# Kernel optimization log

Measured on AMD Instinct MI355X. Metric: run time of the kernel, lower is better.

Reference implementation:

```python
import jax, jax.numpy as jnp
import numpy as np

N, E, G = 40000, 640000, 64
D, H, O = 128, 128, 10
EPS = 1e-5


def _lin(k, fan_in, shape):
    b = 1.0 / np.sqrt(fan_in)
    return jax.random.uniform(k, shape, jnp.float32, -b, b)


def setup_inputs() -> dict:
    key = jax.random.key(0)
    ks = jax.random.split(key, 12)
    x = jax.random.normal(ks[0], (N, D), jnp.float32)
    edge_index = jax.random.randint(ks[1], (2, E), 0, N)
    batch = jnp.sort(jax.random.randint(ks[2], (N,), 0, G))
    return {
        "x": x,
        "edge_index": edge_index,
        "batch": batch,
        "num_graphs": G,
        "W_gcn": _lin(ks[3], D, (D, H)),
        "b_gcn": jnp.zeros((H,), jnp.float32),
        "gamma": jnp.ones((H,), jnp.float32),
        "beta": jnp.zeros((H,), jnp.float32),
        "W1": _lin(ks[4], 3 * H, (3 * H, H)),
        "b1": _lin(ks[5], 3 * H, (H,)),
        "W2": _lin(ks[6], H, (H, H // 2)),
        "b2": _lin(ks[7], H, (H // 2,)),
        "W3": _lin(ks[8], H // 2, (H // 2, O)),
        "b3": _lin(ks[9], H // 2, (O,)),
    }


def reference(x, edge_index, batch, num_graphs, W_gcn, b_gcn, gamma, beta, W1, b1, W2, b2, W3, b3):
    n = x.shape[0]
    src, dst = edge_index[0], edge_index[1]
    # GCNConv: h = D^{-1/2} (A + I) D^{-1/2} (x W) + b  (self-loops, symmetric norm)
    h = x @ W_gcn                                   # [N, H]
    deg = jax.ops.segment_sum(jnp.ones((src.shape[0],), h.dtype), dst, num_segments=n) + 1.0
    dinv = jax.lax.rsqrt(deg)                       # [N]
    coef = dinv[src] * dinv[dst]                    # [E]
    msg = h[src] * coef[:, None]                    # [E, H] gather (memory bound)
    agg = jax.ops.segment_sum(msg, dst, num_segments=n)
    agg = agg + h * (dinv * dinv)[:, None] + b_gcn  # self-loop term + bias
    h = jax.nn.relu(agg)
    # LayerNorm over feature dim
    mu = jnp.mean(h, axis=-1, keepdims=True)
    var = jnp.mean(jnp.square(h - mu), axis=-1, keepdims=True)
    h = (h - mu) * jax.lax.rsqrt(var + EPS) * gamma + beta
    # global mean / add / max pools keyed by graph id
    counts = jax.ops.segment_sum(jnp.ones((n,), h.dtype), batch, num_segments=num_graphs)
    x_add = jax.ops.segment_sum(h, batch, num_segments=num_graphs)
    x_mean = x_add / jnp.maximum(counts, 1.0)[:, None]
    x_max = jax.ops.segment_max(h, batch, num_segments=num_graphs)
    x_max = jnp.where(counts[:, None] > 0, x_max, 0.0)
    g = jnp.concatenate([x_mean, x_add, x_max], axis=1)  # [G, 3H]
    # MLP head (dropout is identity at inference)
    g = jax.nn.relu(g @ W1 + b1)
    g = jax.nn.relu(g @ W2 + b2)
    return g @ W3 + b3
```

## Files before the change

kernel.cpp:

```cpp
#include <hip/hip_runtime.h>
#include <math.h>

#define EPS 1e-5f
#define FLT_BIG 3.402823466e38f

typedef __attribute__((ext_vector_type(8))) short bf16x8;
typedef __attribute__((ext_vector_type(4))) float f32x4;

__device__ __forceinline__ unsigned fflip(float f){
  int i = __float_as_int(f);
  return (unsigned)(i ^ ((i>>31) | 0x80000000));
}
__device__ __forceinline__ float funflip(unsigned u){
  int i = (u & 0x80000000u) ? (int)(u ^ 0x80000000u) : (int)(~u);
  return __int_as_float(i);
}
__device__ __forceinline__ unsigned f2bf(float f){
  unsigned u = __float_as_uint(f);
  return (u + 0x7FFFu + ((u>>16)&1u)) >> 16;
}
__device__ __forceinline__ float bf_lo(unsigned v){ return __uint_as_float(v<<16); }
__device__ __forceinline__ float bf_hi(unsigned v){ return __uint_as_float(v & 0xFFFF0000u); }

__device__ __forceinline__ int lbound(const int* __restrict__ a, int n, int key){
  int lo=0, hi=n;
  while(lo<hi){ int mid=(lo+hi)>>1; if(a[mid]<key) lo=mid+1; else hi=mid; }
  return lo;
}

__global__ __launch_bounds__(256) void k_init(
    int* __restrict__ cursor, int N,
    unsigned* __restrict__ psum, unsigned* __restrict__ pmaxu, int GP,
    const float* __restrict__ Wg, ushort* __restrict__ Wp,
    const int* __restrict__ batch, int* __restrict__ gcnt, int G){
  int i = blockIdx.x*blockDim.x + threadIdx.x;
  if(i<N) cursor[i] = 0;
  if(i<GP){ psum[i]=0u; pmaxu[i]=0u; }
  if(i<G){
    int s = lbound(batch,N,i), e = lbound(batch,N,i+1);
    gcnt[i] = e - s;
  }
  if(i<2048){
    int tile = i>>6, l = i&63;
    int kt = tile>>3, ct = tile&7;
    int q = l>>4, nn = l&15;
    ushort w8[8];
    #pragma unroll
    for(int j=0;j<8;j++)
      w8[j] = (ushort)f2bf(Wg[(kt*32 + q*8 + j)*128 + ct*16 + nn]);
    ushort* dst = Wp + (size_t)i*8;
    #pragma unroll
    for(int j=0;j<8;j++) dst[j] = w8[j];
  }
}

__global__ void k_scatter(const int* __restrict__ src, const int* __restrict__ dst, int E,
                          int* __restrict__ cursor, ushort* __restrict__ csr){
  int i = blockIdx.x*blockDim.x + threadIdx.x;
  int e = i<<2;
  if((E&3)==0){
    if(e<E){
      int4 s4 = *(const int4*)(src+e);
      int4 d4 = *(const int4*)(dst+e);
      int p;
      p = atomicAdd(&cursor[d4.x],1); if(p<64) csr[(d4.x<<6)+p] = (ushort)s4.x;
      p = atomicAdd(&cursor[d4.y],1); if(p<64) csr[(d4.y<<6)+p] = (ushort)s4.y;
      p = atomicAdd(&cursor[d4.z],1); if(p<64) csr[(d4.z<<6)+p] = (ushort)s4.z;
      p = atomicAdd(&cursor[d4.w],1); if(p<64) csr[(d4.w<<6)+p] = (ushort)s4.w;
    }
  } else {
    #pragma unroll
    for(int j=0;j<4;j++){
      int ee = e+j;
      if(ee<E){
        int s = src[ee], d = dst[ee];
        int p = atomicAdd(&cursor[d],1);
        if(p<64) csr[(d<<6)+p] = (ushort)s;
      }
    }
  }
}

__global__ __launch_bounds__(256) void k_scale(
    const float4* __restrict__ x4, int nq, const int* __restrict__ cursor,
    uint2* __restrict__ xs2){
  int i = blockIdx.x*blockDim.x + threadIdx.x;
  if(i>=nq) return;
  int node = i>>5;
  int deg = cursor[node]; if(deg>64) deg=64;
  float dinv = rsqrtf((float)deg + 1.0f);
  float4 v = x4[i];
  uint2 o;
  o.x = (f2bf(v.y*dinv)<<16) | f2bf(v.x*dinv);
  o.y = (f2bf(v.w*dinv)<<16) | f2bf(v.z*dinv);
  xs2[i] = o;
}

__global__ void k_agg(const uint4* __restrict__ xs4, const int* __restrict__ cursor,
                      const ushort* __restrict__ csr, int n, uint4* __restrict__ zb4){
  int w = (blockIdx.x*blockDim.x + threadIdx.x)>>6;
  if(w>=n) return;
  int lane = threadIdx.x & 63;
  int grp = lane>>4, li = lane&15;
  int deg = cursor[w]; if(deg>64) deg=64;
  int k0 = w<<6, k1 = k0+deg;
  float dd = rsqrtf((float)deg + 1.0f);
  float a0=0.f,a1=0.f,a2=0.f,a3=0.f,a4=0.f,a5=0.f,a6=0.f,a7=0.f;
  if(grp==0){
    uint4 sv = xs4[(w<<4)+li];
    a0=bf_lo(sv.x); a1=bf_hi(sv.x); a2=bf_lo(sv.y); a3=bf_hi(sv.y);
    a4=bf_lo(sv.z); a5=bf_hi(sv.z); a6=bf_lo(sv.w); a7=bf_hi(sv.w);
  }
  for(int kb=k0; kb<k1; kb+=16){
    int base = kb + (grp<<2);
    ushort4 s4 = *(const ushort4*)(csr + base);
    if(base   < k1){ uint4 v = xs4[((int)s4.x<<4)+li];
      a0+=bf_lo(v.x); a1+=bf_hi(v.x); a2+=bf_lo(v.y); a3+=bf_hi(v.y);
      a4+=bf_lo(v.z); a5+=bf_hi(v.z); a6+=bf_lo(v.w); a7+=bf_hi(v.w); }
    if(base+1 < k1){ uint4 v = xs4[((int)s4.y<<4)+li];
      a0+=bf_lo(v.x); a1+=bf_hi(v.x); a2+=bf_lo(v.y); a3+=bf_hi(v.y);
      a4+=bf_lo(v.z); a5+=bf_hi(v.z); a6+=bf_lo(v.w); a7+=bf_hi(v.w); }
    if(base+2 < k1){ uint4 v = xs4[((int)s4.z<<4)+li];
      a0+=bf_lo(v.x); a1+=bf_hi(v.x); a2+=bf_lo(v.y); a3+=bf_hi(v.y);
      a4+=bf_lo(v.z); a5+=bf_hi(v.z); a6+=bf_lo(v.w); a7+=bf_hi(v.w); }
    if(base+3 < k1){ uint4 v = xs4[((int)s4.w<<4)+li];
      a0+=bf_lo(v.x); a1+=bf_hi(v.x); a2+=bf_lo(v.y); a3+=bf_hi(v.y);
      a4+=bf_lo(v.z); a5+=bf_hi(v.z); a6+=bf_lo(v.w); a7+=bf_hi(v.w); }
  }
  a0 += __shfl_xor(a0,16,64); a1 += __shfl_xor(a1,16,64);
  a2 += __shfl_xor(a2,16,64); a3 += __shfl_xor(a3,16,64);
  a4 += __shfl_xor(a4,16,64); a5 += __shfl_xor(a5,16,64);
  a6 += __shfl_xor(a6,16,64); a7 += __shfl_xor(a7,16,64);
  a0 += __shfl_xor(a0,32,64); a1 += __shfl_xor(a1,32,64);
  a2 += __shfl_xor(a2,32,64); a3 += __shfl_xor(a3,32,64);
  a4 += __shfl_xor(a4,32,64); a5 += __shfl_xor(a5,32,64);
  a6 += __shfl_xor(a6,32,64); a7 += __shfl_xor(a7,32,64);
  if(grp==0){
    uint4 o;
    o.x = (f2bf(a1*dd)<<16) | f2bf(a0*dd);
    o.y = (f2bf(a3*dd)<<16) | f2bf(a2*dd);
    o.z = (f2bf(a5*dd)<<16) | f2bf(a4*dd);
    o.w = (f2bf(a7*dd)<<16) | f2bf(a6*dd);
    zb4[(w<<4)+li] = o;
  }
}

__global__ __launch_bounds__(256) void k_gemmln(
    const unsigned* __restrict__ zb, const ushort* __restrict__ Wp,
    const float* __restrict__ bgc, const float* __restrict__ gamma, const float* __restrict__ beta,
    const int* __restrict__ batch, int n,
    float* __restrict__ pool_sum, unsigned* __restrict__ pool_maxu){
  __shared__ unsigned ztu[64*68];
  int t = threadIdx.x, lane = t & 63, wv = t >> 6;
  int rowBase = blockIdx.x*64;
  {
    int row = t>>2, qo = (t&3)*16;
    unsigned* lp = ztu + row*68 + qo;
    if(rowBase+row < n){
      const uint4* gp = (const uint4*)(zb + (size_t)(rowBase+row)*64 + qo);
      #pragma unroll
      for(int i=0;i<4;i++) ((uint4*)lp)[i] = gp[i];
    }else{
      #pragma unroll
      for(int i=0;i<4;i++) ((uint4*)lp)[i] = make_uint4(0,0,0,0);
    }
  }
  __syncthreads();

  int q = lane>>4, nn = lane&15;
  int m = wv*16 + nn;
  bf16x8 afr[4];
  #pragma unroll
  for(int kt=0;kt<4;kt++)
    afr[kt] = *(const bf16x8*)((const char*)ztu + m*272 + kt*64 + q*16);

  f32x4 acc[8];
  #pragma unroll
  for(int ct=0;ct<8;ct++){
    f32x4 c = {0.f,0.f,0.f,0.f};
    #pragma unroll
    for(int kt=0;kt<4;kt++){
      bf16x8 bfr = *(const bf16x8*)(Wp + ((size_t)(kt*8+ct)*64 + lane)*8);
      c = __builtin_amdgcn_mfma_f32_16x16x32_bf16(afr[kt], bfr, c, 0, 0, 0);
    }
    acc[ct] = c;
  }
  float s[4]={0,0,0,0}, qq[4]={0,0,0,0};
  #pragma unroll
  for(int ct=0;ct<8;ct++){
    float bb = bgc[ct*16+nn];
    #pragma unroll
    for(int r=0;r<4;r++){
      float v = acc[ct][r] + bb;
      v = fmaxf(v, 0.f);
      acc[ct][r] = v;
      s[r] += v; qq[r] += v*v;
    }
  }
  #pragma unroll
  for(int d=1; d<16; d<<=1){
    #pragma unroll
    for(int r=0;r<4;r++){
      s[r]  += __shfl_xor(s[r],  d, 64);
      qq[r] += __shfl_xor(qq[r], d, 64);
    }
  }
  float mu[4], isd[4];
  #pragma unroll
  for(int r=0;r<4;r++){
    mu[r] = s[r]*(1.f/128.f);
    float var = qq[r]*(1.f/128.f) - mu[r]*mu[r];
    isd[r] = rsqrtf(var + EPS);
  }
  #pragma unroll
  for(int ct=0;ct<8;ct++){
    float gm = gamma[ct*16+nn], bt = beta[ct*16+nn];
    #pragma unroll
    for(int r=0;r<4;r++)
      acc[ct][r] = (acc[ct][r]-mu[r])*isd[r]*gm + bt;
  }
  int gbr[4];
  #pragma unroll
  for(int r=0;r<4;r++){
    int gr = rowBase + wv*16 + q*4 + r;
    gbr[r] = (gr < n) ? batch[gr] : -1;
  }
  int b0i = rowBase + wv*16; if(b0i >= n) b0i = n-1;
  int b15i = rowBase + wv*16 + 15; if(b15i >= n) b15i = n-1;
  int gmin = batch[b0i], gmax = batch[b15i];
  if(gmax < gmin) gmax = gmin;
  for(int g=gmin; g<=gmax; ++g){
    #pragma unroll
    for(int ct=0;ct<8;ct++){
      float ssum = 0.f, smax = -FLT_BIG;
      #pragma unroll
      for(int r=0;r<4;r++){
        if(gbr[r]==g){
          ssum += acc[ct][r];
          smax = fmaxf(smax, acc[ct][r]);
        }
      }
      ssum += __shfl_xor(ssum, 16, 64);
      ssum += __shfl_xor(ssum, 32, 64);
      float o1 = __shfl_xor(smax, 16, 64); smax = fmaxf(smax, o1);
      float o2 = __shfl_xor(smax, 32, 64); smax = fmaxf(smax, o2);
      if(q==0){
        if(ssum != 0.f)     atomicAdd(&pool_sum[g*128 + ct*16 + nn], ssum);
        if(smax > -FLT_BIG) atomicMax(&pool_maxu[g*128 + ct*16 + nn], fflip(smax));
      }
    }
  }
}

__global__ void k_head(const float* __restrict__ pool_sum, const unsigned* __restrict__ pool_maxu,
                       const int* __restrict__ gcnt,
                       const float* __restrict__ W1, const float* __restrict__ b1,
                       const float* __restrict__ W2, const float* __restrict__ b2,
                       const float* __restrict__ W3, const float* __restrict__ b3,
                       float* __restrict__ out){
  int g = blockIdx.x, t = threadIdx.x;
  __shared__ float red[2][128];
  __shared__ float gl[384];
  __shared__ float h1[128];
  __shared__ float h2[64];
  int cnt = gcnt[g];
  if(t<128){
    float s = pool_sum[g*128+t];
    gl[128+t] = s;
    gl[t] = s / (float)((cnt>1)?cnt:1);
    float m = funflip(pool_maxu[g*128+t]);
    gl[256+t] = (cnt>0) ? m : 0.f;
  }
  __syncthreads();
  int j = t & 127, kh = t >> 7;
  float p=0.f;
  for(int k=kh*192; k<kh*192+192; k++) p += gl[k]*W1[k*128+j];
  red[kh][j]=p;
  __syncthreads();
  if(t<128){
    float v = red[0][t]+red[1][t]+b1[t];
    h1[t]=fmaxf(v,0.f);
  }
  __syncthreads();
  if(t<64){
    float a=b2[t];
    for(int k=0;k<128;k++) a += h1[k]*W2[k*64+t];
    h2[t]=fmaxf(a,0.f);
  }
  __syncthreads();
  if(t<10){
    float a=b3[t];
    for(int k=0;k<64;k++) a += h2[k]*W3[k*10+t];
    out[g*10+t]=a;
  }
}

extern "C" void kernel_launch(void* const* d_in, const int* in_sizes, int n_in,
                              void* d_out, int out_size, void* d_ws, size_t ws_size,
                              hipStream_t stream){
  const float* x     = (const float*)d_in[0];
  const int*   ei    = (const int*)d_in[1];
  const int*   batch = (const int*)d_in[2];
  const float* Wg    = (const float*)d_in[4];
  const float* bg    = (const float*)d_in[5];
  const float* gamma = (const float*)d_in[6];
  const float* beta  = (const float*)d_in[7];
  const float* W1    = (const float*)d_in[8];
  const float* b1    = (const float*)d_in[9];
  const float* W2    = (const float*)d_in[10];
  const float* b2    = (const float*)d_in[11];
  const float* W3    = (const float*)d_in[12];
  const float* b3    = (const float*)d_in[13];
  float* out = (float*)d_out;

  int N = in_sizes[0]/128;
  int E = in_sizes[1]/2;
  const int G = 64;
  const int* src = ei;
  const int* dst = ei + E;

  char* p = (char*)d_ws;
  auto alloc=[&](size_t bytes)->char*{ char* r=p; p += (bytes+255)&~(size_t)255; return r; };
  int*      cursor = (int*)     alloc((size_t)N*4);
  ushort*   csr    = (ushort*)  alloc((size_t)N*64*2);
  unsigned* zb     = (unsigned*)alloc((size_t)N*64*4);
  float*    psum   = (float*)   alloc((size_t)G*128*4);
  unsigned* pmaxu  = (unsigned*)alloc((size_t)G*128*4);
  unsigned* xs     = (unsigned*)alloc((size_t)N*64*4);
  ushort*   Wp     = (ushort*)  alloc(2048*8*2);
  int*      gcnt   = (int*)     alloc((size_t)G*4);

  int GP = G*128;
  int nq = N*32;
  int ib = (N+255)/256;
  k_init<<<ib,256,0,stream>>>(cursor,N,(unsigned*)psum,pmaxu,GP,Wg,Wp,batch,gcnt,G);
  int eb = (E/4 + 255)/256;
  k_scatter<<<eb,256,0,stream>>>(src,dst,E,cursor,csr);
  int sb = (nq+255)/256;
  k_scale<<<sb,256,0,stream>>>((const float4*)x,nq,cursor,(uint2*)xs);
  int ab = (int)(((size_t)N*64 + 255)/256);
  k_agg<<<ab,256,0,stream>>>((const uint4*)xs,cursor,csr,N,(uint4*)zb);
  k_gemmln<<<(N+63)/64,256,0,stream>>>(zb,Wp,bg,gamma,beta,batch,N,psum,pmaxu);
  k_head<<<G,256,0,stream>>>(psum,pmaxu,gcnt,W1,b1,W2,b2,W3,b3,out);
}
```

Before: 181.5 us.

## Build CSR via two-pass bucket sort instead of global atomic scatter

Replaces the per-edge global atomicAdd scatter into the padded CSR with a two-stage bucketing scheme. Edges are first grouped by destination block (dst>>8) in shared memory, with one global atomic per bucket per block. A second kernel then builds each 256-node CSR slab in shared memory and writes it out coalesced, also producing the per-node degree counts. The aim is to replace random global atomics and 2-byte scattered stores with shared-memory atomics and coalesced writes, at the cost of an extra kernel launch, an intermediate edge stream, and a fixed cap of 8192 edges per bucket.

After: 170.2 us. -6.2%, faster.

```diff
diff --git a/kernel.cpp b/kernel.cpp
--- a/kernel.cpp
+++ b/kernel.cpp
@@ -29,13 +29,13 @@
 }
 
 __global__ __launch_bounds__(256) void k_init(
-    int* __restrict__ cursor, int N,
     unsigned* __restrict__ psum, unsigned* __restrict__ pmaxu, int GP,
     const float* __restrict__ Wg, ushort* __restrict__ Wp,
-    const int* __restrict__ batch, int* __restrict__ gcnt, int G){
+    const int* __restrict__ batch, int N, int* __restrict__ gcnt, int G,
+    unsigned* __restrict__ gcur, int NB){
   int i = blockIdx.x*blockDim.x + threadIdx.x;
-  if(i<N) cursor[i] = 0;
   if(i<GP){ psum[i]=0u; pmaxu[i]=0u; }
+  if(i<NB) gcur[i]=0u;
   if(i<G){
     int s = lbound(batch,N,i), e = lbound(batch,N,i+1);
     gcnt[i] = e - s;
@@ -54,31 +54,100 @@
   }
 }
 
-__global__ void k_scatter(const int* __restrict__ src, const int* __restrict__ dst, int E,
-                          int* __restrict__ cursor, ushort* __restrict__ csr){
-  int i = blockIdx.x*blockDim.x + threadIdx.x;
-  int e = i<<2;
-  if((E&3)==0){
-    if(e<E){
-      int4 s4 = *(const int4*)(src+e);
-      int4 d4 = *(const int4*)(dst+e);
-      int p;
-      p = atomicAdd(&cursor[d4.x],1); if(p<64) csr[(d4.x<<6)+p] = (ushort)s4.x;
-      p = atomicAdd(&cursor[d4.y],1); if(p<64) csr[(d4.y<<6)+p] = (ushort)s4.y;
-      p = atomicAdd(&cursor[d4.z],1); if(p<64) csr[(d4.z<<6)+p] = (ushort)s4.z;
-      p = atomicAdd(&cursor[d4.w],1); if(p<64) csr[(d4.w<<6)+p] = (ushort)s4.w;
+__global__ __launch_bounds__(256) void k_bucketize(
+    const int* __restrict__ src, const int* __restrict__ dst, int E, int NB,
+    unsigned* __restrict__ gcur, unsigned* __restrict__ dstream){
+  __shared__ unsigned hist[160];
+  __shared__ unsigned scan[256];
+  __shared__ unsigned excl[160];
+  __shared__ unsigned base[160];
+  __shared__ unsigned lsorted[2048];
+  int t = threadIdx.x, bid = blockIdx.x;
+  int e0 = bid*2048 + t*8;
+  unsigned rec[8]; int bk[8]; unsigned rr[8];
+  #pragma unroll
+  for(int j=0;j<8;j++) bk[j] = -1;
+  if(e0+7 < E){
+    int4 s0 = *(const int4*)(src+e0), s1 = *(const int4*)(src+e0+4);
+    int4 d0 = *(const int4*)(dst+e0), d1 = *(const int4*)(dst+e0+4);
+    int ss[8] = {s0.x,s0.y,s0.z,s0.w,s1.x,s1.y,s1.z,s1.w};
+    int dd[8] = {d0.x,d0.y,d0.z,d0.w,d1.x,d1.y,d1.z,d1.w};
+    #pragma unroll
+    for(int j=0;j<8;j++){
+      bk[j] = dd[j]>>8;
+      rec[j] = ((unsigned)bk[j]<<24) | ((unsigned)(dd[j]&255)<<16) | (unsigned)ss[j];
     }
   } else {
     #pragma unroll
-    for(int j=0;j<4;j++){
-      int ee = e+j;
+    for(int j=0;j<8;j++){
+      int ee = e0+j;
       if(ee<E){
         int s = src[ee], d = dst[ee];
-        int p = atomicAdd(&cursor[d],1);
-        if(p<64) csr[(d<<6)+p] = (ushort)s;
+        bk[j] = d>>8;
+        rec[j] = ((unsigned)bk[j]<<24) | ((unsigned)(d&255)<<16) | (unsigned)s;
       }
     }
   }
+  for(int i=t;i<NB;i+=256) hist[i]=0u;
+  __syncthreads();
+  #pragma unroll
+  for(int j=0;j<8;j++)
+    if(bk[j]>=0) rr[j] = atomicAdd(&hist[bk[j]],1u);
+  __syncthreads();
+  unsigned hv = (t<NB)?hist[t]:0u;
+  scan[t]=hv;
+  __syncthreads();
+  #pragma unroll
+  for(int off=1; off<256; off<<=1){
+    unsigned v = scan[t]; if(t>=off) v += scan[t-off];
+    __syncthreads(); scan[t]=v; __syncthreads();
+  }
+  if(t<NB){
+    excl[t] = scan[t]-hv;
+    int ridx = t + bid; while(ridx>=NB) ridx-=NB;
+    base[ridx] = atomicAdd(&gcur[ridx], hist[ridx]);
+  }
+  __syncthreads();
+  #pragma unroll
+  for(int j=0;j<8;j++)
+    if(bk[j]>=0) lsorted[excl[bk[j]]+rr[j]] = rec[j];
+  __syncthreads();
+  int vc = E - bid*2048; if(vc>2048) vc=2048;
+  #pragma unroll
+  for(int j=0;j<8;j++){
+    int k = j*256 + t;
+    if(k<vc){
+      unsigned rc = lsorted[k];
+      unsigned bb = rc>>24;
+      unsigned pos = base[bb] + (unsigned)k - excl[bb];
+      if(pos < 8192u) dstream[((size_t)bb<<13) + pos] = rc;
+    }
+  }
+}
+
+__global__ __launch_bounds__(256) void k_csr(
+    const unsigned* __restrict__ dstream, const unsigned* __restrict__ gcur,
+    int N, ushort* __restrict__ csr, int* __restrict__ cursor){
+  __shared__ unsigned cnt[256];
+  __shared__ ushort slab[16384];
+  int b = blockIdx.x, t = threadIdx.x;
+  cnt[t]=0u;
+  __syncthreads();
+  int nb = (int)gcur[b]; if(nb>8192) nb=8192;
+  const unsigned* sp = dstream + ((size_t)b<<13);
+  for(int i=t;i<nb;i+=256){
+    unsigned rc = sp[i];
+    int dl = (rc>>16)&255;
+    unsigned p = atomicAdd(&cnt[dl],1u);
+    if(p<64u) slab[(dl<<6)+(int)p] = (ushort)(rc & 0xFFFFu);
+  }
+  __syncthreads();
+  const uint4* s4 = (const uint4*)slab;
+  uint4* c4 = ((uint4*)csr) + ((size_t)b<<11);
+  #pragma unroll
+  for(int i=t;i<2048;i+=256) c4[i] = s4[i];
+  int node = (b<<8) + t;
+  if(node<N) cursor[node] = (int)cnt[t];
 }
 
 __global__ __launch_bounds__(256) void k_scale(
@@ -318,24 +387,27 @@
   const int G = 64;
   const int* src = ei;
   const int* dst = ei + E;
+  int NB = (N+255)>>8;
 
   char* p = (char*)d_ws;
   auto alloc=[&](size_t bytes)->char*{ char* r=p; p += (bytes+255)&~(size_t)255; return r; };
-  int*      cursor = (int*)     alloc((size_t)N*4);
-  ushort*   csr    = (ushort*)  alloc((size_t)N*64*2);
-  unsigned* zb     = (unsigned*)alloc((size_t)N*64*4);
-  float*    psum   = (float*)   alloc((size_t)G*128*4);
-  unsigned* pmaxu  = (unsigned*)alloc((size_t)G*128*4);
-  unsigned* xs     = (unsigned*)alloc((size_t)N*64*4);
-  ushort*   Wp     = (ushort*)  alloc(2048*8*2);
-  int*      gcnt   = (int*)     alloc((size_t)G*4);
+  int*      cursor  = (int*)     alloc((size_t)N*4);
+  ushort*   csr     = (ushort*)  alloc((size_t)NB*16384*2);
+  unsigned* zb      = (unsigned*)alloc((size_t)N*64*4);
+  float*    psum    = (float*)   alloc((size_t)G*128*4);
+  unsigned* pmaxu   = (unsigned*)alloc((size_t)G*128*4);
+  unsigned* xs      = (unsigned*)alloc((size_t)N*64*4);
+  ushort*   Wp      = (ushort*)  alloc(2048*8*2);
+  int*      gcnt    = (int*)     alloc((size_t)G*4);
+  unsigned* gcur    = (unsigned*)alloc((size_t)NB*4);
+  unsigned* dstream = (unsigned*)alloc((size_t)NB*8192*4);
 
   int GP = G*128;
   int nq = N*32;
-  int ib = (N+255)/256;
-  k_init<<<ib,256,0,stream>>>(cursor,N,(unsigned*)psum,pmaxu,GP,Wg,Wp,batch,gcnt,G);
-  int eb = (E/4 + 255)/256;
-  k_scatter<<<eb,256,0,stream>>>(src,dst,E,cursor,csr);
+  k_init<<<32,256,0,stream>>>((unsigned*)psum,pmaxu,GP,Wg,Wp,batch,N,gcnt,G,gcur,NB);
+  int bb = (E+2047)/2048;
+  k_bucketize<<<bb,256,0,stream>>>(src,dst,E,NB,gcur,dstream);
+  k_csr<<<NB,256,0,stream>>>(dstream,gcur,N,csr,cursor);
   int sb = (nq+255)/256;
   k_scale<<<sb,256,0,stream>>>((const float4*)x,nq,cursor,(uint2*)xs);
   int ab = (int)(((size_t)N*64 + 255)/256);
```
